# Kernel tuning notes

Hardware: AMD Instinct MI355X
Metric: run time of the kernel (lower is better)

The kernel has to match this reference:

```python
import jax, jax.numpy as jnp
import numpy as np

B, L, F2, T, D, H = 128, 196, 512, 32, 256, 512


def setup_inputs() -> dict:
    key = jax.random.key(0)
    ks = jax.random.split(key, 12)
    g = lambda k, sh, s: (jax.random.normal(k, sh, dtype=jnp.float32) * s)
    return {
        "input_data": g(ks[0], (B, L, F2), 1.0),
        "word_inputs": g(ks[1], (B, T, D), 1.0),
        # init-state projections (glorot-ish scale)
        "w_h": g(ks[2], (F2, H), 0.04),
        "b_h": jnp.zeros((H,), jnp.float32),
        "w_c": g(ks[3], (F2, H), 0.04),
        "b_c": jnp.zeros((H,), jnp.float32),
        # simple additive attention (L2Attention=False, Gatted=False)
        "w_a_h": g(ks[4], (H, 1), 0.06),
        "w_a": g(ks[5], (F2, 1), 0.06),
        "b_a": jnp.zeros((1,), jnp.float32),
        # keras LSTMCell params: kernel [D+F2, 4H], recurrent [H, 4H], bias [4H]
        "lstm_kernel": g(ks[6], (D + F2, 4 * H), 0.03),
        "lstm_recurrent": g(ks[7], (H, 4 * H), 0.03),
        "lstm_bias": jnp.zeros((4 * H,), jnp.float32),
    }


def reference(input_data, word_inputs, w_h, b_h, w_c, b_c, w_a_h, w_a, b_a,
              lstm_kernel, lstm_recurrent, lstm_bias):
    # initial states from mean-pooled features
    features_mean = jnp.mean(input_data, axis=1)          # [B, F2]
    h = jnp.tanh(features_mean @ w_h + b_h)               # [B, H]
    c = jnp.tanh(features_mean @ w_c + b_c)               # [B, H]

    # time-invariant part of the attention score: input_data @ w_a -> [B, L]
    feat_score = jnp.einsum('blf,fo->blo', input_data, w_a)[..., 0] + b_a[0]

    def step(carry, word_t):
        h, c = carry
        # additive attention: tanh(h@w_a_h [B,1] + feat_score [B,L]) -> softmax over L
        score = jnp.tanh((h @ w_a_h) + feat_score)        # [B, L]
        alfa = jax.nn.softmax(score, axis=-1)             # [B, L]
        context = jnp.einsum('blf,bl->bf', input_data, alfa)  # [B, F2]
        # keras LSTMCell: gate order i, f, g(cell), o
        x = jnp.concatenate([word_t, context], axis=1)    # [B, D+F2]
        z = x @ lstm_kernel + h @ lstm_recurrent + lstm_bias
        i, f, g, o = jnp.split(z, 4, axis=-1)
        c_new = jax.nn.sigmoid(f) * c + jax.nn.sigmoid(i) * jnp.tanh(g)
        h_new = jax.nn.sigmoid(o) * jnp.tanh(c_new)
        return (h_new, c_new), (h_new, c_new, alfa)

    (_, _), (hs, cs, alfas) = jax.lax.scan(step, (h, c), jnp.swapaxes(word_inputs, 0, 1))
    hiddens = jnp.swapaxes(hs, 0, 1)   # [B, T, H]
    memory = cs                        # [T, B, H] (original returns a list of T [B,H] tensors)
    alfas = jnp.swapaxes(alfas, 0, 1)  # [B, T, L]
    return hiddens, memory, alfas
```

## Files before the change

### kernel.cpp

```cpp
#include <hip/hip_runtime.h>
#include <math.h>

#define B  128
#define L  196
#define F2 512
#define T  32
#define D  256
#define H  512
#define H4 2048
#define KCAT 1280
#define KS 4
#define KCHUNK 320

typedef __attribute__((ext_vector_type(8))) short bf16x8;
typedef __attribute__((ext_vector_type(4))) float f32x4;

__device__ __forceinline__ float sigf(float x) { return 1.0f / (1.0f + expf(-x)); }
__device__ __forceinline__ unsigned short f2bf(float x) {
    unsigned u = __float_as_uint(x);
    u += 0x7FFF + ((u >> 16) & 1);
    return (unsigned short)(u >> 16);
}
__device__ __forceinline__ float bf2f(unsigned short s) {
    return __uint_as_float(((unsigned)s) << 16);
}
__device__ __forceinline__ float wred_sum(float v) {
    for (int o = 32; o > 0; o >>= 1) v += __shfl_down(v, o);
    return v;
}
__device__ __forceinline__ float wred_max(float v) {
    for (int o = 32; o > 0; o >>= 1) v = fmaxf(v, __shfl_down(v, o));
    return v;
}


__global__ void k_prep2(const float* __restrict__ X, const float* __restrict__ w_a,
                        const float* __restrict__ b_a, unsigned short* __restrict__ Xb,
                        float* __restrict__ fscore, float* __restrict__ fmpart) {
    __shared__ float sp[8][512];
    int b = blockIdx.x, g = blockIdx.y, tid = threadIdx.x;
    int rowi = tid >> 5, lane32 = tid & 31;
    int f0 = tid * 2;
    float2 acc = make_float2(0.f, 0.f);
    for (int s = 0; s < 4; ++s) {
        int li = s * 8 + rowi;
        float4 part[4];
        if (li < 28) {
            size_t row = (size_t)b * L + g * 28 + li;
            const float* src = X + row * F2;
            unsigned short* dst = Xb + row * F2;
            float sc = 0.f;
            #pragma unroll
            for (int j = 0; j < 4; ++j) {
                int f = j * 128 + lane32 * 4;
                float4 v = *(const float4*)(src + f);
                float4 w = *(const float4*)(w_a + f);
                sc += v.x * w.x + v.y * w.y + v.z * w.z + v.w * w.w;
                part[j] = v;
                ushort4 u;
                u.x = f2bf(v.x); u.y = f2bf(v.y); u.z = f2bf(v.z); u.w = f2bf(v.w);
                *(ushort4*)(dst + f) = u;
            }
            for (int o = 16; o > 0; o >>= 1) sc += __shfl_down(sc, o, 32);
            if (lane32 == 0) fscore[row] = sc + b_a[0];
        } else {
            #pragma unroll
            for (int j = 0; j < 4; ++j) part[j] = make_float4(0.f, 0.f, 0.f, 0.f);
        }
        __syncthreads();
        #pragma unroll
        for (int j = 0; j < 4; ++j)
            *(float4*)&sp[rowi][j * 128 + lane32 * 4] = part[j];
        __syncthreads();
        #pragma unroll
        for (int r = 0; r < 8; ++r) { acc.x += sp[r][f0]; acc.y += sp[r][f0 + 1]; }
    }
    *(float2*)&fmpart[((size_t)b * 7 + g) * 512 + f0] = acc;
}

__global__ void k_mred(const float* __restrict__ fmpart, unsigned short* __restrict__ fmb) {
    int b = blockIdx.x, tid = threadIdx.x;
    int f0 = tid * 2;
    float2 acc = make_float2(0.f, 0.f);
    #pragma unroll
    for (int g = 0; g < 7; ++g) {
        float2 v = *(const float2*)&fmpart[((size_t)b * 7 + g) * 512 + f0];
        acc.x += v.x; acc.y += v.y;
    }
    ushort2 u; u.x = f2bf(acc.x * (1.0f / L)); u.y = f2bf(acc.y * (1.0f / L));
    *(ushort2*)(fmb + (size_t)b * F2 + f0) = u;
}

__global__ void k_castw(const float* __restrict__ src, unsigned short* __restrict__ dst) {
    size_t i = ((size_t)blockIdx.x * 256 + threadIdx.x) * 8;
    float4 v0 = *(const float4*)(src + i);
    float4 v1 = *(const float4*)(src + i + 4);
    ushort4 u0, u1;
    u0.x = f2bf(v0.x); u0.y = f2bf(v0.y); u0.z = f2bf(v0.z); u0.w = f2bf(v0.w);
    u1.x = f2bf(v1.x); u1.y = f2bf(v1.y); u1.z = f2bf(v1.z); u1.w = f2bf(v1.w);
    *(ushort4*)(dst + i) = u0;
    *(ushort4*)(dst + i + 4) = u1;
}

__global__ void k_trW(const float* __restrict__ k_w, const float* __restrict__ r_w,
                      unsigned short* __restrict__ WcatT) {
    int job = blockIdx.z;
    if (job == 2 && blockIdx.x >= 8) return;
    const float* src; int colOff;
    if (job == 0)      { src = k_w + (size_t)256 * H4; colOff = 0; }
    else if (job == 1) { src = r_w;                    colOff = 512; }
    else               { src = k_w;                    colOff = 1024; }
    __shared__ float Ls[32][65];
    int r0 = blockIdx.x * 32, c0 = blockIdx.y * 64;
    int tid = threadIdx.x;
    int r = tid >> 3, c8 = (tid & 7) * 8;
    const float* s = src + (size_t)(r0 + r) * H4 + c0 + c8;
    #pragma unroll
    for (int j = 0; j < 8; ++j) Ls[r][c8 + j] = s[j];
    __syncthreads();
    int cc = tid >> 2, q = tid & 3;
    unsigned short tmp[8];
    #pragma unroll
    for (int j = 0; j < 8; ++j) tmp[j] = f2bf(Ls[q * 8 + j][cc]);
    *(float4*)(WcatT + (size_t)(c0 + cc) * KCAT + colOff + r0 + q * 8) = *(float4*)tmp;
}

__global__ void k_trI(const float* __restrict__ w_h, const float* __restrict__ w_c,
                      unsigned short* __restrict__ wiT) {
    int job = blockIdx.z;
    const float* src = job ? w_c : w_h;
    unsigned short* dst = wiT + (size_t)job * 512 * 512;
    __shared__ float Ls[32][65];
    int r0 = blockIdx.x * 32, c0 = blockIdx.y * 64;
    int tid = threadIdx.x;
    int r = tid >> 3, c8 = (tid & 7) * 8;
    const float* s = src + (size_t)(r0 + r) * 512 + c0 + c8;
    #pragma unroll
    for (int j = 0; j < 8; ++j) Ls[r][c8 + j] = s[j];
    __syncthreads();
    int cc = tid >> 2, q = tid & 3;
    unsigned short tmp[8];
    #pragma unroll
    for (int j = 0; j < 8; ++j) tmp[j] = f2bf(Ls[q * 8 + j][cc]);
    *(float4*)(dst + (size_t)(c0 + cc) * 512 + r0 + q * 8) = *(float4*)tmp;
}

__global__ __launch_bounds__(256) void k_init_gemm(
    const unsigned short* __restrict__ A,
    const unsigned short* __restrict__ Bt,
    const float* __restrict__ b_h, const float* __restrict__ b_c,
    unsigned short* __restrict__ Abuf0, float* __restrict__ cbuf) {
    __shared__ short As[128 * 64];
    __shared__ short Bs[128 * 64];
    int tid = threadIdx.x;
    int nbase = blockIdx.x * 128;
    int wave = tid >> 6, lane = tid & 63;
    int wm = (wave >> 1) * 64, wn = (wave & 1) * 64;
    int l15 = lane & 15, l4 = lane >> 4;

    f32x4 acc[4][4];
    #pragma unroll
    for (int i = 0; i < 4; ++i)
        #pragma unroll
        for (int j = 0; j < 4; ++j) acc[i][j] = (f32x4){0.f, 0.f, 0.f, 0.f};

    for (int it = 0; it < 8; ++it) {
        int kbase = it * 64;
        #pragma unroll
        for (int ch = 0; ch < 4; ++ch) {
            int idx = ch * 256 + tid;
            int row = idx >> 3, q = idx & 7;
            int k = kbase + q * 8;
            float4 v = *(const float4*)(A + (size_t)row * 512 + k);
            *(float4*)&As[row * 64 + ((q ^ (row & 7)) << 3)] = v;
            float4 w = *(const float4*)(Bt + (size_t)(nbase + row) * 512 + k);
            *(float4*)&Bs[row * 64 + ((q ^ (row & 7)) << 3)] = w;
        }
        __syncthreads();
        #pragma unroll
        for (int ks = 0; ks < 2; ++ks) {
            bf16x8 a[4], b[4];
            #pragma unroll
            for (int f = 0; f < 4; ++f) {
                int ar = wm + f * 16 + l15;
                int q = ks * 4 + l4;
                a[f] = *(const bf16x8*)&As[ar * 64 + ((q ^ (ar & 7)) << 3)];
                int br = wn + f * 16 + l15;
                b[f] = *(const bf16x8*)&Bs[br * 64 + ((q ^ (br & 7)) << 3)];
            }
            #pragma unroll
            for (int fm = 0; fm < 4; ++fm)
                #pragma unroll
                for (int fn = 0; fn < 4; ++fn)
                    acc[fm][fn] = __builtin_amdgcn_mfma_f32_16x16x32_bf16(a[fm], b[fn], acc[fm][fn], 0, 0, 0);
        }
        __syncthreads();
    }
    #pragma unroll
    for (int fm = 0; fm < 4; ++fm)
        #pragma unroll
        for (int j = 0; j < 4; ++j) {
            int m = wm + fm * 16 + l4 * 4 + j;
            #pragma unroll
            for (int fn = 0; fn < 4; ++fn) {
                int gn = nbase + wn + fn * 16 + l15;
                float v = acc[fm][fn][j];
                if (gn < 512) Abuf0[(size_t)m * 1024 + 512 + gn] = f2bf(tanhf(v + b_h[gn]));
                else          cbuf[(size_t)m * 512 + gn - 512] = tanhf(v + b_c[gn - 512]);
            }
        }
}

__global__ __launch_bounds__(256) void k_gemm32(
    const unsigned short* __restrict__ Abuf, const unsigned short* __restrict__ wordb,
    const unsigned short* __restrict__ WcatT, float* __restrict__ zpart, int t) {
    __shared__ short As[64 * 64];
    __shared__ short Bs[32 * 64];
    int tid = threadIdx.x;
    int bid = blockIdx.x;
    int ksb = bid >> 7, rem = bid & 127;
    int rowbase = (rem >> 6) * 64, nbase = (rem & 63) * 32;
    int wave = tid >> 6, lane = tid & 63;
    int wm = (wave & 1) * 32, wn = (wave >> 1) * 16;
    int l15 = lane & 15, l4 = lane >> 4;

    f32x4 acc[2];
    acc[0] = (f32x4){0.f, 0.f, 0.f, 0.f};
    acc[1] = (f32x4){0.f, 0.f, 0.f, 0.f};

    for (int it = 0; it < KCHUNK / 64; ++it) {
        int kbase = ksb * KCHUNK + it * 64;
        #pragma unroll
        for (int p = 0; p < 2; ++p) {
            int idx = p * 256 + tid;
            int row = idx >> 3, q = idx & 7;
            int k = kbase + q * 8;
            int gr = rowbase + row;
            float4 v;
            if (k < 1024) v = *(const float4*)(Abuf + (size_t)gr * 1024 + k);
            else          v = *(const float4*)(wordb + ((size_t)gr * T + t) * D + (k - 1024));
            *(float4*)&As[row * 64 + ((q ^ (row & 7)) << 3)] = v;
        }
        {
            int row = tid >> 3, q = tid & 7;
            float4 w = *(const float4*)(WcatT + (size_t)(nbase + row) * KCAT + kbase + q * 8);
            *(float4*)&Bs[row * 64 + ((q ^ (row & 7)) << 3)] = w;
        }
        __syncthreads();
        #pragma unroll
        for (int ks2 = 0; ks2 < 2; ++ks2) {
            int q = ks2 * 4 + l4;
            bf16x8 a[2], bb;
            #pragma unroll
            for (int fm = 0; fm < 2; ++fm) {
                int ar = wm + fm * 16 + l15;
                a[fm] = *(const bf16x8*)&As[ar * 64 + ((q ^ (ar & 7)) << 3)];
            }
            {
                int br = wn + l15;
                bb = *(const bf16x8*)&Bs[br * 64 + ((q ^ (br & 7)) << 3)];
            }
            #pragma unroll
            for (int fm = 0; fm < 2; ++fm)
                acc[fm] = __builtin_amdgcn_mfma_f32_16x16x32_bf16(a[fm], bb, acc[fm], 0, 0, 0);
        }
        __syncthreads();
    }
    float* zp = zpart + (size_t)ksb * B * H4;
    #pragma unroll
    for (int fm = 0; fm < 2; ++fm)
        #pragma unroll
        for (int j = 0; j < 4; ++j) {
            int m = rowbase + wm + fm * 16 + l4 * 4 + j;
            zp[(size_t)m * H4 + nbase + wn + l15] = acc[fm][j];
        }
}

__global__ __launch_bounds__(256) void k_step4(
    const float* __restrict__ zpart, const float* __restrict__ bias,
    const float* __restrict__ cb_cur, float* __restrict__ cb_nxt,
    unsigned short* __restrict__ Abuf,
    const unsigned short* __restrict__ Xb, const float* __restrict__ fscore,
    const float* __restrict__ w_a_h,
    float* __restrict__ out_h, float* __restrict__ out_m, float* __restrict__ out_a,
    int t_next) {
    __shared__ float red[12];
    __shared__ float sal[200];
    __shared__ float sp2[4][64][2];
    int b = blockIdx.x, quarter = blockIdx.y, tid = threadIdx.x;
    int lane = tid & 63, wid = tid >> 6;
    int n0 = tid * 2;
    float hp;
    if (t_next > 0) {
        float2 z[4];
        #pragma unroll
        for (int g = 0; g < 4; ++g) z[g] = *(const float2*)(bias + g * H + n0);
        #pragma unroll
        for (int ks = 0; ks < KS; ++ks) {
            const float* zp = zpart + ((size_t)ks * B + b) * H4;
            #pragma unroll
            for (int g = 0; g < 4; ++g) {
                float2 v = *(const float2*)(zp + g * H + n0);
                z[g].x += v.x; z[g].y += v.y;
            }
        }
        float2 cv = *(const float2*)(cb_cur + (size_t)b * H + n0);
        float cnx = sigf(z[1].x) * cv.x + sigf(z[0].x) * tanhf(z[2].x);
        float cny = sigf(z[1].y) * cv.y + sigf(z[0].y) * tanhf(z[2].y);
        float hnx = sigf(z[3].x) * tanhf(cnx);
        float hny = sigf(z[3].y) * tanhf(cny);
        if (quarter == 0) {
            int tp = t_next - 1;
            *(float2*)(cb_nxt + (size_t)b * H + n0) = make_float2(cnx, cny);
            *(float2*)(out_m + ((size_t)tp * B + b) * H + n0) = make_float2(cnx, cny);
            *(float2*)(out_h + ((size_t)b * T + tp) * H + n0) = make_float2(hnx, hny);
            ushort2 hu; hu.x = f2bf(hnx); hu.y = f2bf(hny);
            *(ushort2*)(Abuf + (size_t)b * 1024 + 512 + n0) = hu;
        }
        hp = hnx * w_a_h[n0] + hny * w_a_h[n0 + 1];
    } else {
        ushort2 hu = *(const ushort2*)(Abuf + (size_t)b * 1024 + 512 + n0);
        hp = bf2f(hu.x) * w_a_h[n0] + bf2f(hu.y) * w_a_h[n0 + 1];
    }
    if (t_next >= T) return;

    float s = wred_sum(hp);
    if (lane == 0) red[wid] = s;
    __syncthreads();
    float hs = red[0] + red[1] + red[2] + red[3];
    float scv = (tid < L) ? tanhf(hs + fscore[b * L + tid]) : -3.0e38f;
    float m = wred_max(scv);
    if (lane == 0) red[4 + wid] = m;
    __syncthreads();
    float mx = fmaxf(fmaxf(red[4], red[5]), fmaxf(red[6], red[7]));
    float ex = (tid < L) ? expf(scv - mx) : 0.f;
    float es = wred_sum(ex);
    if (lane == 0) red[8 + wid] = es;
    __syncthreads();
    float denom = red[8] + red[9] + red[10] + red[11];
    float al = ex / denom;
    if (tid < L) {
        sal[tid] = al;
        if (quarter == 0) out_a[((size_t)b * T + t_next) * L + tid] = al;
    }
    __syncthreads();

    int fi = tid & 63, lg = tid >> 6;
    const unsigned* xb32 = (const unsigned*)(Xb + (size_t)b * L * F2) + quarter * 64 + fi;
    int l0 = lg * 49;
    float a0 = 0.f, a1 = 0.f;
    for (int sblk = 0; sblk < 49; sblk += 7) {
        unsigned u[7];
        #pragma unroll
        for (int j = 0; j < 7; ++j) u[j] = xb32[(size_t)(l0 + sblk + j) * 256];
        #pragma unroll
        for (int j = 0; j < 7; ++j) {
            float w = sal[l0 + sblk + j];
            a0 += bf2f((unsigned short)(u[j] & 0xFFFF)) * w;
            a1 += bf2f((unsigned short)(u[j] >> 16)) * w;
        }
    }
    sp2[lg][fi][0] = a0; sp2[lg][fi][1] = a1;
    __syncthreads();
    if (tid < 64) {
        ushort2 cu;
        cu.x = f2bf(sp2[0][tid][0] + sp2[1][tid][0] + sp2[2][tid][0] + sp2[3][tid][0]);
        cu.y = f2bf(sp2[0][tid][1] + sp2[1][tid][1] + sp2[2][tid][1] + sp2[3][tid][1]);
        *(ushort2*)(Abuf + (size_t)b * 1024 + (quarter * 64 + tid) * 2) = cu;
    }
}

extern "C" void kernel_launch(void* const* d_in, const int* in_sizes, int n_in,
                              void* d_out, int out_size, void* d_ws, size_t ws_size,
                              hipStream_t stream) {
    (void)in_sizes; (void)n_in; (void)out_size; (void)ws_size;
    const float* X     = (const float*)d_in[0];
    const float* word  = (const float*)d_in[1];
    const float* w_h   = (const float*)d_in[2];
    const float* b_h   = (const float*)d_in[3];
    const float* w_c   = (const float*)d_in[4];
    const float* b_c   = (const float*)d_in[5];
    const float* w_a_h = (const float*)d_in[6];
    const float* w_a   = (const float*)d_in[7];
    const float* b_a   = (const float*)d_in[8];
    const float* k_w   = (const float*)d_in[9];
    const float* r_w   = (const float*)d_in[10];
    const float* bias  = (const float*)d_in[11];

    float* out_h = (float*)d_out;
    float* out_m = out_h + (size_t)B * T * H;
    float* out_a = out_m + (size_t)T * B * H;

    char* p = (char*)d_ws;
    unsigned short* Xb    = (unsigned short*)p; p += (size_t)B * L * F2 * 2;
    unsigned short* WcatT = (unsigned short*)p; p += (size_t)H4 * KCAT * 2;
    unsigned short* wiT   = (unsigned short*)p; p += (size_t)1024 * 512 * 2;
    unsigned short* wordb = (unsigned short*)p; p += (size_t)B * T * D * 2;
    unsigned short* fmb   = (unsigned short*)p; p += (size_t)B * F2 * 2;
    unsigned short* Abuf  = (unsigned short*)p; p += (size_t)B * 1024 * 2;
    float* fscore = (float*)p; p += (size_t)B * L * 4;
    float* cb0    = (float*)p; p += (size_t)B * H * 4;
    float* cb1    = (float*)p; p += (size_t)B * H * 4;
    float* zpart  = (float*)p; p += (size_t)KS * B * H4 * 4;
    float* fmpart = zpart;

    k_prep2<<<dim3(B, 7), 256, 0, stream>>>(X, w_a, b_a, Xb, fscore, fmpart);
    k_mred<<<B, 256, 0, stream>>>(fmpart, fmb);
    k_castw<<<512, 256, 0, stream>>>(word, wordb);
    k_trW<<<dim3(16, 32, 3), 256, 0, stream>>>(k_w, r_w, WcatT);
    k_trI<<<dim3(16, 8, 2), 256, 0, stream>>>(w_h, w_c, wiT);
    k_init_gemm<<<8, 256, 0, stream>>>(fmb, wiT, b_h, b_c, Abuf, cb0);

    float* cb[2] = {cb0, cb1};
    k_step4<<<dim3(B, 4), 256, 0, stream>>>(zpart, bias, cb0, cb1, Abuf, Xb,
                                            fscore, w_a_h, out_h, out_m, out_a, 0);
    for (int t = 0; t < T; ++t) {
        k_gemm32<<<512, 256, 0, stream>>>(Abuf, wordb, WcatT, zpart, t);
        k_step4<<<dim3(B, 4), 256, 0, stream>>>(zpart, bias, cb[t & 1], cb[(t + 1) & 1],
                                                Abuf, Xb, fscore, w_a_h,
                                                out_h, out_m, out_a, t + 1);
    }
}
```

Baseline: 512.5 us.

## Double-buffer LDS tiles in step GEMM and drop softmax max reduction

```diff
diff --git a/kernel.cpp b/kernel.cpp
--- a/kernel.cpp
+++ b/kernel.cpp
@@ -26,10 +26,6 @@
 }
 __device__ __forceinline__ float wred_sum(float v) {
     for (int o = 32; o > 0; o >>= 1) v += __shfl_down(v, o);
-    return v;
-}
-__device__ __forceinline__ float wred_max(float v) {
-    for (int o = 32; o > 0; o >>= 1) v = fmaxf(v, __shfl_down(v, o));
     return v;
 }
 
@@ -146,8 +142,7 @@
 }
 
 __global__ __launch_bounds__(256) void k_init_gemm(
-    const unsigned short* __restrict__ A,
-    const unsigned short* __restrict__ Bt,
+    const unsigned short* __restrict__ A, const unsigned short* __restrict__ Bt,
     const float* __restrict__ b_h, const float* __restrict__ b_c,
     unsigned short* __restrict__ Abuf0, float* __restrict__ cbuf) {
     __shared__ short As[128 * 64];
@@ -214,8 +209,8 @@
 __global__ __launch_bounds__(256) void k_gemm32(
     const unsigned short* __restrict__ Abuf, const unsigned short* __restrict__ wordb,
     const unsigned short* __restrict__ WcatT, float* __restrict__ zpart, int t) {
-    __shared__ short As[64 * 64];
-    __shared__ short Bs[32 * 64];
+    __shared__ short As[2][64 * 64];
+    __shared__ short Bs[2][32 * 64];
     int tid = threadIdx.x;
     int bid = blockIdx.x;
     int ksb = bid >> 7, rem = bid & 127;
@@ -224,29 +219,48 @@
     int wm = (wave & 1) * 32, wn = (wave >> 1) * 16;
     int l15 = lane & 15, l4 = lane >> 4;
 
+    int arow = tid >> 3, aq = tid & 7;
+    int brow = tid >> 3, bq = tid & 7;
+
     f32x4 acc[2];
     acc[0] = (f32x4){0.f, 0.f, 0.f, 0.f};
     acc[1] = (f32x4){0.f, 0.f, 0.f, 0.f};
 
+    float4 va[2], wb;
+    {
+        int kbase = ksb * KCHUNK;
+        #pragma unroll
+        for (int p = 0; p < 2; ++p) {
+            int row = (p * 256 + tid) >> 3;
+            int k = kbase + aq * 8;
+            int gr = rowbase + row;
+            if (k < 1024) va[p] = *(const float4*)(Abuf + (size_t)gr * 1024 + k);
+            else          va[p] = *(const float4*)(wordb + ((size_t)gr * T + t) * D + (k - 1024));
+        }
+        wb = *(const float4*)(WcatT + (size_t)(nbase + brow) * KCAT + kbase + bq * 8);
+    }
+    #pragma unroll
+    for (int p = 0; p < 2; ++p) {
+        int row = (p * 256 + tid) >> 3;
+        *(float4*)&As[0][row * 64 + ((aq ^ (row & 7)) << 3)] = va[p];
+    }
+    *(float4*)&Bs[0][brow * 64 + ((bq ^ (brow & 7)) << 3)] = wb;
+
+    int cur = 0;
     for (int it = 0; it < KCHUNK / 64; ++it) {
-        int kbase = ksb * KCHUNK + it * 64;
-        #pragma unroll
-        for (int p = 0; p < 2; ++p) {
-            int idx = p * 256 + tid;
-            int row = idx >> 3, q = idx & 7;
-            int k = kbase + q * 8;
-            int gr = rowbase + row;
-            float4 v;
-            if (k < 1024) v = *(const float4*)(Abuf + (size_t)gr * 1024 + k);
-            else          v = *(const float4*)(wordb + ((size_t)gr * T + t) * D + (k - 1024));
-            *(float4*)&As[row * 64 + ((q ^ (row & 7)) << 3)] = v;
-        }
-        {
-            int row = tid >> 3, q = tid & 7;
-            float4 w = *(const float4*)(WcatT + (size_t)(nbase + row) * KCAT + kbase + q * 8);
-            *(float4*)&Bs[row * 64 + ((q ^ (row & 7)) << 3)] = w;
-        }
         __syncthreads();
+        if (it < KCHUNK / 64 - 1) {
+            int kbase = ksb * KCHUNK + (it + 1) * 64;
+            #pragma unroll
+            for (int p = 0; p < 2; ++p) {
+                int row = (p * 256 + tid) >> 3;
+                int k = kbase + aq * 8;
+                int gr = rowbase + row;
+                if (k < 1024) va[p] = *(const float4*)(Abuf + (size_t)gr * 1024 + k);
+                else          va[p] = *(const float4*)(wordb + ((size_t)gr * T + t) * D + (k - 1024));
+            }
+            wb = *(const float4*)(WcatT + (size_t)(nbase + brow) * KCAT + kbase + bq * 8);
+        }
         #pragma unroll
         for (int ks2 = 0; ks2 < 2; ++ks2) {
             int q = ks2 * 4 + l4;
@@ -254,17 +268,25 @@
             #pragma unroll
             for (int fm = 0; fm < 2; ++fm) {
                 int ar = wm + fm * 16 + l15;
-                a[fm] = *(const bf16x8*)&As[ar * 64 + ((q ^ (ar & 7)) << 3)];
+                a[fm] = *(const bf16x8*)&As[cur][ar * 64 + ((q ^ (ar & 7)) << 3)];
             }
             {
                 int br = wn + l15;
-                bb = *(const bf16x8*)&Bs[br * 64 + ((q ^ (br & 7)) << 3)];
+                bb = *(const bf16x8*)&Bs[cur][br * 64 + ((q ^ (br & 7)) << 3)];
             }
             #pragma unroll
             for (int fm = 0; fm < 2; ++fm)
                 acc[fm] = __builtin_amdgcn_mfma_f32_16x16x32_bf16(a[fm], bb, acc[fm], 0, 0, 0);
         }
-        __syncthreads();
+        if (it < KCHUNK / 64 - 1) {
+            #pragma unroll
+            for (int p = 0; p < 2; ++p) {
+                int row = (p * 256 + tid) >> 3;
+                *(float4*)&As[cur ^ 1][row * 64 + ((aq ^ (row & 7)) << 3)] = va[p];
+            }
+            *(float4*)&Bs[cur ^ 1][brow * 64 + ((bq ^ (brow & 7)) << 3)] = wb;
+            cur ^= 1;
+        }
     }
     float* zp = zpart + (size_t)ksb * B * H4;
     #pragma unroll
@@ -284,7 +306,7 @@
     const float* __restrict__ w_a_h,
     float* __restrict__ out_h, float* __restrict__ out_m, float* __restrict__ out_a,
     int t_next) {
-    __shared__ float red[12];
+    __shared__ float red[8];
     __shared__ float sal[200];
     __shared__ float sp2[4][64][2];
     int b = blockIdx.x, quarter = blockIdx.y, tid = threadIdx.x;
@@ -328,16 +350,12 @@
     if (lane == 0) red[wid] = s;
     __syncthreads();
     float hs = red[0] + red[1] + red[2] + red[3];
-    float scv = (tid < L) ? tanhf(hs + fscore[b * L + tid]) : -3.0e38f;
-    float m = wred_max(scv);
-    if (lane == 0) red[4 + wid] = m;
-    __syncthreads();
-    float mx = fmaxf(fmaxf(red[4], red[5]), fmaxf(red[6], red[7]));
-    float ex = (tid < L) ? expf(scv - mx) : 0.f;
+    float scv = (tid < L) ? tanhf(hs + fscore[b * L + tid]) : 0.f;
+    float ex = (tid < L) ? expf(scv) : 0.f;
     float es = wred_sum(ex);
-    if (lane == 0) red[8 + wid] = es;
-    __syncthreads();
-    float denom = red[8] + red[9] + red[10] + red[11];
+    if (lane == 0) red[4 + wid] = es;
+    __syncthreads();
+    float denom = red[4] + red[5] + red[6] + red[7];
     float al = ex / denom;
     if (tid < L) {
         sal[tid] = al;
```

Result: slower. 555.7 us (+8.4%).
